# Kernel tuning notes

Measured on AMD Instinct MI355X. Metric: run time of the kernel, lower is better.

## Reference

```python
import jax, jax.numpy as jnp
import numpy as np

D_MODEL = 1024
D_STATE = 16
BATCH = 4
SEQLEN = 4096


def setup_inputs() -> dict:
    key = jax.random.key(0)
    kx, kA, kB, kC = jax.random.split(key, 4)
    x = jax.random.normal(kx, (BATCH, SEQLEN, D_MODEL), dtype=jnp.float32)
    # Params per init_weights(): A ~ N(-0.5, 0.1), B ~ N(0, 0.1), C ~ N(0, 0.1), D = 0
    A = -0.5 + 0.1 * jax.random.normal(kA, (1, D_STATE), dtype=jnp.float32)
    B_in = 0.1 * jax.random.normal(kB, (D_MODEL, D_STATE), dtype=jnp.float32)
    C = 0.1 * jax.random.normal(kC, (D_STATE, D_MODEL), dtype=jnp.float32)
    D = jnp.zeros((D_MODEL,), dtype=jnp.float32)
    return {"x": x, "A": A, "B_in": B_in, "C": C, "D": D}


def reference(x, A, B_in, C, D):
    # x: [B, N, E]; A: [1, S]; B_in: [E, S]; C: [S, E]; D: [E]
    A_neg = -jnp.exp(A)                              # [1, S]
    Bx = jnp.einsum('bne,es->bns', x, B_in)          # [B, N, S] = x @ B
    delta = jax.nn.softplus(Bx)                      # softplus(u @ B)
    decay = jnp.exp(delta * A_neg)                   # [B, N, S]

    def step(h, inp):
        d_t, bx_t = inp                              # each [B, S]
        h = h * d_t + bx_t
        return h, h

    h0 = jnp.zeros((x.shape[0], A.shape[1]), dtype=x.dtype)
    # scan over time: inputs [N, B, S]
    _, hs = jax.lax.scan(step, h0, (decay.transpose(1, 0, 2), Bx.transpose(1, 0, 2)))
    # readout: y_t = h_t @ C + x_t * D  (dropout p=0.0 -> identity)
    y = jnp.einsum('nbs,se->bne', hs, C) + x * D
    return y
```

## Files before the change

kernel.cpp:

```cpp
#include <hip/hip_runtime.h>

#define NSEQ 4096
#define EDIM 1024

#define OFF_PBX 0u
#define OFF_HT  524288u

__device__ __forceinline__ void fma4(float4& a, float xv, const float4& b) {
    a.x = fmaf(xv, b.x, a.x);
    a.y = fmaf(xv, b.y, a.y);
    a.z = fmaf(xv, b.z, a.z);
    a.w = fmaf(xv, b.w, a.w);
}

__global__ __launch_bounds__(256, 2) void k1_bx(const float* __restrict__ x,
                                                const float* __restrict__ Bin,
                                                float* __restrict__ ws) {
    __shared__ float smem[2 * 64 * 132];

    const int tid  = threadIdx.x;
    const int lane = tid & 63;
    const int wu   = __builtin_amdgcn_readfirstlane(tid) >> 6;
    const int r0   = (blockIdx.x >> 1) * 64;
    const int eh   = blockIdx.x & 1;
    const int b    = r0 >> 12;
    const int n0   = r0 & 4095;

    const float4* xf4 = (const float4*)x;
    const float4* Bf4 = (const float4*)Bin;

    float acc[16];
#pragma unroll
    for (int s = 0; s < 16; s++) acc[s] = 0.f;

    float4 pf[8];
#pragma unroll
    for (int k = 0; k < 8; k++) {
        int i = tid + 256 * k, row = i >> 5, c4 = i & 31;
        pf[k] = xf4[(size_t)(r0 + row) * 256 + eh * 128 + c4];
    }

    for (int c = 0; c < 4; ++c) {
        float* stg = &smem[(c & 1) * 8448];
#pragma unroll
        for (int k = 0; k < 8; k++) {
            int i = tid + 256 * k, row = i >> 5, c4 = i & 31;
            *(float4*)&stg[row * 132 + c4 * 4] = pf[k];
        }
        if (c < 3) {
#pragma unroll
            for (int k = 0; k < 8; k++) {
                int i = tid + 256 * k, row = i >> 5, c4 = i & 31;
                pf[k] = xf4[(size_t)(r0 + row) * 256 + eh * 128 + (c + 1) * 32 + c4];
            }
        }
        __syncthreads();

#pragma unroll
        for (int j4 = 0; j4 < 8; j4++) {
            const float4 xq = *(const float4*)&stg[lane * 132 + wu * 32 + j4 * 4];
#pragma unroll
            for (int jj = 0; jj < 4; jj++) {
                const int e = eh * 512 + c * 128 + wu * 32 + j4 * 4 + jj;
                const float4 b0 = Bf4[e * 4 + 0];
                const float4 b1 = Bf4[e * 4 + 1];
                const float4 b2 = Bf4[e * 4 + 2];
                const float4 b3 = Bf4[e * 4 + 3];
                const float xv = (jj == 0) ? xq.x : (jj == 1) ? xq.y
                                : (jj == 2) ? xq.z : xq.w;
                acc[0]  = fmaf(xv, b0.x, acc[0]);  acc[1]  = fmaf(xv, b0.y, acc[1]);
                acc[2]  = fmaf(xv, b0.z, acc[2]);  acc[3]  = fmaf(xv, b0.w, acc[3]);
                acc[4]  = fmaf(xv, b1.x, acc[4]);  acc[5]  = fmaf(xv, b1.y, acc[5]);
                acc[6]  = fmaf(xv, b1.z, acc[6]);  acc[7]  = fmaf(xv, b1.w, acc[7]);
                acc[8]  = fmaf(xv, b2.x, acc[8]);  acc[9]  = fmaf(xv, b2.y, acc[9]);
                acc[10] = fmaf(xv, b2.z, acc[10]); acc[11] = fmaf(xv, b2.w, acc[11]);
                acc[12] = fmaf(xv, b3.x, acc[12]); acc[13] = fmaf(xv, b3.y, acc[13]);
                acc[14] = fmaf(xv, b3.z, acc[14]); acc[15] = fmaf(xv, b3.w, acc[15]);
            }
        }
        __syncthreads();
    }

    {
        const int rb = (wu * 64 + lane) * 17;
#pragma unroll
        for (int s = 0; s < 16; s++) smem[rb + s] = acc[s];
    }
    __syncthreads();

#pragma unroll
    for (int q = 0; q < 4; q++) {
        const int o   = tid + 256 * q;
        const int s   = o >> 6;
        const int row = o & 63;
        const float v = smem[(0 * 64 + row) * 17 + s] + smem[(1 * 64 + row) * 17 + s] +
                        smem[(2 * 64 + row) * 17 + s] + smem[(3 * 64 + row) * 17 + s];
        ws[OFF_PBX + eh * 262144u + (size_t)(b * 16 + s) * NSEQ + n0 + row] = v;
    }
}

__global__ __launch_bounds__(256) void k2_scan(const float* __restrict__ A,
                                               float* __restrict__ ws) {
    __shared__ float sP[4], sH[4];
    const int tid   = threadIdx.x;
    const int lane  = tid & 63;
    const int w     = tid >> 6;
    const int chain = blockIdx.x;
    const int bb    = chain >> 4, ss = chain & 15;

    const float4* P0 = (const float4*)(ws + OFF_PBX) + (size_t)chain * 1024;
    const float4* P1 = (const float4*)(ws + OFF_PBX + 262144u) + (size_t)chain * 1024;

    float bx[16], de[16];
    const float Ae = expf(A[ss]);
#pragma unroll
    for (int k = 0; k < 4; k++) {
        float4 a0 = P0[tid * 4 + k], a1 = P1[tid * 4 + k];
        float vv[4] = {a0.x + a1.x, a0.y + a1.y, a0.z + a1.z, a0.w + a1.w};
#pragma unroll
        for (int j = 0; j < 4; j++) {
            float v  = vv[j];
            float sp = fmaxf(v, 0.f) + log1pf(expf(-fabsf(v)));
            bx[k * 4 + j] = v;
            de[k * 4 + j] = expf(-Ae * sp);
        }
    }

    float P = 1.f, h = 0.f;
#pragma unroll
    for (int k = 0; k < 16; k++) { h = fmaf(h, de[k], bx[k]); P *= de[k]; }

    float Pi = P, hi = h;
#pragma unroll
    for (int off = 1; off < 64; off <<= 1) {
        float Pp = __shfl_up(Pi, off, 64);
        float hp = __shfl_up(hi, off, 64);
        if (lane >= off) { hi = fmaf(hp, Pi, hi); Pi *= Pp; }
    }

    if (lane == 63) { sP[w] = Pi; sH[w] = hi; }
    __syncthreads();

    float hw = 0.f;
    for (int q = 0; q < w; q++) hw = fmaf(hw, sP[q], sH[q]);

    float Pe = __shfl_up(Pi, 1, 64);
    float he = __shfl_up(hi, 1, 64);
    if (lane == 0) { Pe = 1.f; he = 0.f; }
    float hr = fmaf(hw, Pe, he);

    float* htp = ws + OFF_HT + ((size_t)bb * NSEQ + tid * 16) * 16 + ss;
#pragma unroll
    for (int k = 0; k < 16; k++) {
        hr = fmaf(hr, de[k], bx[k]);
        htp[k * 16] = hr;
    }
}

__global__ __launch_bounds__(256) void k3_out(const float* __restrict__ x,
                                              const float* __restrict__ C,
                                              const float* __restrict__ D,
                                              const float* __restrict__ ws,
                                              float* __restrict__ out) {
    const int tid = threadIdx.x;
    const int blk = blockIdx.x;
    const int tc  = blk & 255;
    const int b   = blk >> 8;
    const int t0  = tc * 16;

    const float4* C4 = (const float4*)C;
    float4 creg[16];
#pragma unroll
    for (int s = 0; s < 16; s++) creg[s] = C4[s * 256 + tid];
    float4 dreg = ((const float4*)D)[tid];

    const bool needX = __any((dreg.x != 0.f) | (dreg.y != 0.f) |
                             (dreg.z != 0.f) | (dreg.w != 0.f));

    const float* hb = ws + OFF_HT + ((size_t)b * NSEQ + t0) * 16;

    const float4* x4 = (const float4*)x;
    float4* o4 = (float4*)out;
    const size_t rowbase = ((size_t)b * NSEQ + t0) * 256;

    if (needX) {
#pragma unroll 4
        for (int tt = 0; tt < 16; tt++) {
            float4 xv = x4[rowbase + tt * 256 + tid];
            float4 y;
            y.x = xv.x * dreg.x; y.y = xv.y * dreg.y;
            y.z = xv.z * dreg.z; y.w = xv.w * dreg.w;
#pragma unroll
            for (int s = 0; s < 16; s++) fma4(y, hb[tt * 16 + s], creg[s]);
            o4[rowbase + tt * 256 + tid] = y;
        }
    } else {
#pragma unroll 4
        for (int tt = 0; tt < 16; tt++) {
            float4 y = make_float4(0.f, 0.f, 0.f, 0.f);
#pragma unroll
            for (int s = 0; s < 16; s++) fma4(y, hb[tt * 16 + s], creg[s]);
            o4[rowbase + tt * 256 + tid] = y;
        }
    }
}

extern "C" void kernel_launch(void* const* d_in, const int* in_sizes, int n_in,
                              void* d_out, int out_size, void* d_ws, size_t ws_size,
                              hipStream_t stream) {
    const float* x   = (const float*)d_in[0];
    const float* A   = (const float*)d_in[1];
    const float* Bin = (const float*)d_in[2];
    const float* C   = (const float*)d_in[3];
    const float* D   = (const float*)d_in[4];
    float* out = (float*)d_out;
    float* ws  = (float*)d_ws;

    hipLaunchKernelGGL(k1_bx,   dim3(512),  dim3(256), 0, stream, x, Bin, ws);
    hipLaunchKernelGGL(k2_scan, dim3(64),   dim3(256), 0, stream, A, ws);
    hipLaunchKernelGGL(k3_out,  dim3(1024), dim3(256), 0, stream, x, C, D, ws, out);
}
```

Baseline: 162.0 us.

## Split Bx projection into four E-quarters with smaller padded LDS tiles

```diff
diff --git a/kernel.cpp b/kernel.cpp
--- a/kernel.cpp
+++ b/kernel.cpp
@@ -4,7 +4,7 @@
 #define EDIM 1024
 
 #define OFF_PBX 0u
-#define OFF_HT  524288u
+#define OFF_HT  1048576u
 
 __device__ __forceinline__ void fma4(float4& a, float xv, const float4& b) {
     a.x = fmaf(xv, b.x, a.x);
@@ -13,18 +13,19 @@
     a.w = fmaf(xv, b.w, a.w);
 }
 
-__global__ __launch_bounds__(256, 2) void k1_bx(const float* __restrict__ x,
+__global__ __launch_bounds__(256, 4) void k1_bx(const float* __restrict__ x,
                                                 const float* __restrict__ Bin,
                                                 float* __restrict__ ws) {
-    __shared__ float smem[2 * 64 * 132];
+    __shared__ float smem[2 * 64 * 65];
 
     const int tid  = threadIdx.x;
     const int lane = tid & 63;
     const int wu   = __builtin_amdgcn_readfirstlane(tid) >> 6;
-    const int r0   = (blockIdx.x >> 1) * 64;
-    const int eh   = blockIdx.x & 1;
+    const int q    = blockIdx.x & 3;
+    const int r0   = (blockIdx.x >> 2) * 64;
     const int b    = r0 >> 12;
     const int n0   = r0 & 4095;
+    const int eq   = q * 256;
 
     const float4* xf4 = (const float4*)x;
     const float4* Bf4 = (const float4*)Bin;
@@ -33,49 +34,59 @@
 #pragma unroll
     for (int s = 0; s < 16; s++) acc[s] = 0.f;
 
-    float4 pf[8];
-#pragma unroll
-    for (int k = 0; k < 8; k++) {
-        int i = tid + 256 * k, row = i >> 5, c4 = i & 31;
-        pf[k] = xf4[(size_t)(r0 + row) * 256 + eh * 128 + c4];
-    }
+    float4 pf[4];
+#pragma unroll
+    for (int k = 0; k < 4; k++) {
+        int i = tid + 256 * k, row = i >> 4, cq = i & 15;
+        pf[k] = xf4[(size_t)(r0 + row) * 256 + q * 64 + cq];
+    }
+    {
+        float* stg = smem;
+#pragma unroll
+        for (int k = 0; k < 4; k++) {
+            int i = tid + 256 * k, row = i >> 4, cq = i & 15;
+            float* p = &stg[row * 65 + cq * 4];
+            p[0] = pf[k].x; p[1] = pf[k].y; p[2] = pf[k].z; p[3] = pf[k].w;
+        }
+    }
+    __syncthreads();
 
     for (int c = 0; c < 4; ++c) {
-        float* stg = &smem[(c & 1) * 8448];
-#pragma unroll
-        for (int k = 0; k < 8; k++) {
-            int i = tid + 256 * k, row = i >> 5, c4 = i & 31;
-            *(float4*)&stg[row * 132 + c4 * 4] = pf[k];
-        }
         if (c < 3) {
 #pragma unroll
-            for (int k = 0; k < 8; k++) {
-                int i = tid + 256 * k, row = i >> 5, c4 = i & 31;
-                pf[k] = xf4[(size_t)(r0 + row) * 256 + eh * 128 + (c + 1) * 32 + c4];
+            for (int k = 0; k < 4; k++) {
+                int i = tid + 256 * k, row = i >> 4, cq = i & 15;
+                pf[k] = xf4[(size_t)(r0 + row) * 256 + q * 64 + (c + 1) * 16 + cq];
             }
         }
-        __syncthreads();
-
-#pragma unroll
-        for (int j4 = 0; j4 < 8; j4++) {
-            const float4 xq = *(const float4*)&stg[lane * 132 + wu * 32 + j4 * 4];
-#pragma unroll
-            for (int jj = 0; jj < 4; jj++) {
-                const int e = eh * 512 + c * 128 + wu * 32 + j4 * 4 + jj;
-                const float4 b0 = Bf4[e * 4 + 0];
-                const float4 b1 = Bf4[e * 4 + 1];
-                const float4 b2 = Bf4[e * 4 + 2];
-                const float4 b3 = Bf4[e * 4 + 3];
-                const float xv = (jj == 0) ? xq.x : (jj == 1) ? xq.y
-                                : (jj == 2) ? xq.z : xq.w;
-                acc[0]  = fmaf(xv, b0.x, acc[0]);  acc[1]  = fmaf(xv, b0.y, acc[1]);
-                acc[2]  = fmaf(xv, b0.z, acc[2]);  acc[3]  = fmaf(xv, b0.w, acc[3]);
-                acc[4]  = fmaf(xv, b1.x, acc[4]);  acc[5]  = fmaf(xv, b1.y, acc[5]);
-                acc[6]  = fmaf(xv, b1.z, acc[6]);  acc[7]  = fmaf(xv, b1.w, acc[7]);
-                acc[8]  = fmaf(xv, b2.x, acc[8]);  acc[9]  = fmaf(xv, b2.y, acc[9]);
-                acc[10] = fmaf(xv, b2.z, acc[10]); acc[11] = fmaf(xv, b2.w, acc[11]);
-                acc[12] = fmaf(xv, b3.x, acc[12]); acc[13] = fmaf(xv, b3.y, acc[13]);
-                acc[14] = fmaf(xv, b3.z, acc[14]); acc[15] = fmaf(xv, b3.w, acc[15]);
+
+        const float* stg = &smem[(c & 1) * 4160];
+#pragma unroll
+        for (int j = 0; j < 16; ++j) {
+            const int el = wu * 16 + j;
+            const int e  = eq + c * 64 + el;
+            const float4 b0 = Bf4[e * 4 + 0];
+            const float4 b1 = Bf4[e * 4 + 1];
+            const float4 b2 = Bf4[e * 4 + 2];
+            const float4 b3 = Bf4[e * 4 + 3];
+            const float xv = stg[lane * 65 + el];
+            acc[0]  = fmaf(xv, b0.x, acc[0]);  acc[1]  = fmaf(xv, b0.y, acc[1]);
+            acc[2]  = fmaf(xv, b0.z, acc[2]);  acc[3]  = fmaf(xv, b0.w, acc[3]);
+            acc[4]  = fmaf(xv, b1.x, acc[4]);  acc[5]  = fmaf(xv, b1.y, acc[5]);
+            acc[6]  = fmaf(xv, b1.z, acc[6]);  acc[7]  = fmaf(xv, b1.w, acc[7]);
+            acc[8]  = fmaf(xv, b2.x, acc[8]);  acc[9]  = fmaf(xv, b2.y, acc[9]);
+            acc[10] = fmaf(xv, b2.z, acc[10]); acc[11] = fmaf(xv, b2.w, acc[11]);
+            acc[12] = fmaf(xv, b3.x, acc[12]); acc[13] = fmaf(xv, b3.y, acc[13]);
+            acc[14] = fmaf(xv, b3.z, acc[14]); acc[15] = fmaf(xv, b3.w, acc[15]);
+        }
+
+        if (c < 3) {
+            float* dst = &smem[((c + 1) & 1) * 4160];
+#pragma unroll
+            for (int k = 0; k < 4; k++) {
+                int i = tid + 256 * k, row = i >> 4, cq = i & 15;
+                float* p = &dst[row * 65 + cq * 4];
+                p[0] = pf[k].x; p[1] = pf[k].y; p[2] = pf[k].z; p[3] = pf[k].w;
             }
         }
         __syncthreads();
@@ -89,13 +100,13 @@
     __syncthreads();
 
 #pragma unroll
-    for (int q = 0; q < 4; q++) {
-        const int o   = tid + 256 * q;
+    for (int p = 0; p < 4; p++) {
+        const int o   = tid + 256 * p;
         const int s   = o >> 6;
         const int row = o & 63;
         const float v = smem[(0 * 64 + row) * 17 + s] + smem[(1 * 64 + row) * 17 + s] +
                         smem[(2 * 64 + row) * 17 + s] + smem[(3 * 64 + row) * 17 + s];
-        ws[OFF_PBX + eh * 262144u + (size_t)(b * 16 + s) * NSEQ + n0 + row] = v;
+        ws[OFF_PBX + (size_t)q * 262144u + (size_t)(b * 16 + s) * NSEQ + n0 + row] = v;
     }
 }
 
@@ -108,15 +119,19 @@
     const int chain = blockIdx.x;
     const int bb    = chain >> 4, ss = chain & 15;
 
-    const float4* P0 = (const float4*)(ws + OFF_PBX) + (size_t)chain * 1024;
-    const float4* P1 = (const float4*)(ws + OFF_PBX + 262144u) + (size_t)chain * 1024;
-
     float bx[16], de[16];
     const float Ae = expf(A[ss]);
 #pragma unroll
     for (int k = 0; k < 4; k++) {
-        float4 a0 = P0[tid * 4 + k], a1 = P1[tid * 4 + k];
-        float vv[4] = {a0.x + a1.x, a0.y + a1.y, a0.z + a1.z, a0.w + a1.w};
+        float4 v4 = make_float4(0.f, 0.f, 0.f, 0.f);
+#pragma unroll
+        for (int q = 0; q < 4; q++) {
+            const float4* Pq = (const float4*)(ws + OFF_PBX + (size_t)q * 262144u +
+                                               (size_t)chain * NSEQ);
+            float4 a = Pq[tid * 4 + k];
+            v4.x += a.x; v4.y += a.y; v4.z += a.z; v4.w += a.w;
+        }
+        float vv[4] = {v4.x, v4.y, v4.z, v4.w};
 #pragma unroll
         for (int j = 0; j < 4; j++) {
             float v  = vv[j];
@@ -142,7 +157,7 @@
     __syncthreads();
 
     float hw = 0.f;
-    for (int q = 0; q < w; q++) hw = fmaf(hw, sP[q], sH[q]);
+    for (int qq = 0; qq < w; qq++) hw = fmaf(hw, sP[qq], sH[qq]);
 
     float Pe = __shfl_up(Pi, 1, 64);
     float he = __shfl_up(hi, 1, 64);
@@ -216,7 +231,7 @@
     float* out = (float*)d_out;
     float* ws  = (float*)d_ws;
 
-    hipLaunchKernelGGL(k1_bx,   dim3(512),  dim3(256), 0, stream, x, Bin, ws);
+    hipLaunchKernelGGL(k1_bx,   dim3(1024), dim3(256), 0, stream, x, Bin, ws);
     hipLaunchKernelGGL(k2_scan, dim3(64),   dim3(256), 0, stream, A, ws);
     hipLaunchKernelGGL(k3_out,  dim3(1024), dim3(256), 0, stream, x, C, D, ws, out);
 }
```

Measured after the change: 140.2 us. 1.16x faster.
